# Performance work log

Measured on AMD Instinct MI355X. Metric: run time of the kernel, lower is better.

## Reference

```python
import jax, jax.numpy as jnp
import numpy as np

B, S, D, H = 4, 2048, 1024, 16
HD = D // H


def setup_inputs() -> dict:
    key = jax.random.key(0)
    ks = jax.random.split(key, 9)
    s = 0.02  # GPT-2 init scale for weights
    return {
        "hidden_states": jax.random.normal(ks[0], (B, S, D), jnp.float32),
        "Wq": jax.random.normal(ks[1], (D, D), jnp.float32) * s,
        "bq": jnp.zeros((D,), jnp.float32),
        "Wk": jax.random.normal(ks[2], (D, D), jnp.float32) * s,
        "bk": jnp.zeros((D,), jnp.float32),
        "Wv": jax.random.normal(ks[3], (D, D), jnp.float32) * s,
        "bv": jnp.zeros((D,), jnp.float32),
        "Wo": jax.random.normal(ks[4], (D, D), jnp.float32) * s,
        "bo": jnp.zeros((D,), jnp.float32),
    }


def _split_heads(x):
    b, s, _ = x.shape
    return x.reshape(b, s, H, HD).transpose(0, 2, 1, 3)  # [B,H,S,HD]


def reference(hidden_states, Wq, bq, Wk, bk, Wv, bv, Wo, bo):
    b, s, d = hidden_states.shape
    q = _split_heads(hidden_states @ Wq + bq)
    k = _split_heads(hidden_states @ Wk + bk)
    v = _split_heads(hidden_states @ Wv + bv)
    # naive attention: full [B,H,S,S] scores, scale, causal where-mask, softmax, AV
    scores = jnp.einsum('bhqd,bhkd->bhqk', q, k)
    scores = scores / jnp.asarray(HD, scores.dtype) ** 0.5  # scale_attn_weights
    causal = jnp.tril(jnp.ones((s, s), dtype=bool))  # bias buffer slice
    scores = jnp.where(causal, scores, jnp.finfo(scores.dtype).min)
    attn = jax.nn.softmax(scores, axis=-1)  # attn_dropout p=0 -> identity
    out = jnp.einsum('bhqk,bhkd->bhqd', attn, v)
    out = out.transpose(0, 2, 1, 3).reshape(b, s, d)  # merge heads
    return out @ Wo + bo  # resid_dropout p=0 -> identity
```

## Files before the change

### kernel.cpp

```cpp
#include <hip/hip_runtime.h>
#include <stdint.h>


#define GAS __attribute__((address_space(1)))
#define LAS __attribute__((address_space(3)))

typedef __attribute__((ext_vector_type(4))) float f32x4;
typedef __attribute__((ext_vector_type(8))) short bf16x8;

__device__ __forceinline__ short f2bf(float f) {
  union { float f; uint32_t u; } v; v.f = f;
  uint32_t r = v.u + 0x7fffu + ((v.u >> 16) & 1u);
  return (short)(r >> 16);
}

__device__ __forceinline__ float bf2f(short s) {
  union { uint32_t u; float f; } v;
  v.u = ((uint32_t)(uint16_t)s) << 16;
  return v.f;
}

__device__ __forceinline__ uint32_t cvt_pk_bf16(float lo, float hi) {
  uint32_t r;
  asm("v_cvt_pk_bf16_f32 %0, %1, %2" : "=v"(r) : "v"(lo), "v"(hi));
  return r;
}

__device__ __forceinline__ void gload_lds16(const void* g, void* l) {
  __builtin_amdgcn_global_load_lds((const GAS void*)g, (LAS void*)l, 16, 0, 0);
}

#define GATE(N)                                            \
  __builtin_amdgcn_sched_barrier(0);                       \
  asm volatile("s_waitcnt vmcnt(" #N ")" ::: "memory");    \
  __builtin_amdgcn_s_barrier();                            \
  __builtin_amdgcn_sched_barrier(0);

__global__ __launch_bounds__(256) void cvt_bf16_kernel(const float* __restrict__ in,
                                                       short* __restrict__ out, int n4) {
  int i = blockIdx.x * blockDim.x + threadIdx.x;
  int stride = gridDim.x * blockDim.x;
  for (int idx = i; idx < n4; idx += stride) {
    float4 v = ((const float4*)in)[idx];
    short4 o;
    o.x = f2bf(v.x); o.y = f2bf(v.y); o.z = f2bf(v.z); o.w = f2bf(v.w);
    ((short4*)out)[idx] = o;
  }
}

__global__ __launch_bounds__(256) void wt4_kernel(const float* __restrict__ W0,
                                                  const float* __restrict__ W1,
                                                  const float* __restrict__ W2,
                                                  const float* __restrict__ W3,
                                                  short* __restrict__ Wt) {
  __shared__ short tile[64][65];
  const float* W = (blockIdx.z == 0) ? W0 : (blockIdx.z == 1) ? W1
                   : (blockIdx.z == 2) ? W2 : W3;
  short* dst = Wt + ((size_t)blockIdx.z << 20);
  const int k0 = blockIdx.x * 64, n0 = blockIdx.y * 64;
  const int t = threadIdx.x;
#pragma unroll
  for (int i = 0; i < 16; ++i) {
    int r = (t >> 6) + i * 4, c = t & 63;
    tile[r][c] = f2bf(W[(size_t)(k0 + r) * 1024 + n0 + c]);
  }
  __syncthreads();
#pragma unroll
  for (int i = 0; i < 16; ++i) {
    int r = (t >> 6) + i * 4, c = t & 63;
    dst[(size_t)(n0 + r) * 1024 + k0 + c] = tile[c][r];
  }
}

template <int MODE>
__global__ __launch_bounds__(256, 4) void gemmS(const short* __restrict__ A,
                                                const short* __restrict__ Bt,
                                                const float* __restrict__ b0,
                                                const float* __restrict__ b1,
                                                const float* __restrict__ b2,
                                                void* __restrict__ O0,
                                                void* __restrict__ O1,
                                                void* __restrict__ O2) {
  __shared__ short lds[2][8192];
  const int xcd = (int)blockIdx.x & 7;
  const int t = (int)blockIdx.x >> 3;
  const int m0 = (xcd * 8 + (t & 7)) * 128;
  const int n0 = (t >> 3) * 128;
  const int tid = threadIdx.x;
  const int lane = tid & 63, w = tid >> 6;
  const int l15 = lane & 15, lg = lane >> 4;
  const int wm = w >> 1, wn = w & 1;

  const short* ag[2];
  const short* bg[2];
#pragma unroll
  for (int i = 0; i < 2; ++i) {
    const int P = w * 64 + i * 256 + lane;
    const int L = P ^ ((P >> 3) & 7);
    ag[i] = A + (size_t)(m0 + (L >> 2)) * 1024 + (L & 3) * 8;
    bg[i] = Bt + (size_t)(n0 + (L >> 2)) * 1024 + (L & 3) * 8;
  }

  int aof[4], bof[4];
#pragma unroll
  for (int mf = 0; mf < 4; ++mf) {
    const int L = (wm * 64 + mf * 16 + l15) * 4 + lg;
    aof[mf] = (L ^ ((L >> 3) & 7)) * 8;
  }
#pragma unroll
  for (int nf = 0; nf < 4; ++nf) {
    const int L = (wn * 64 + nf * 16 + l15) * 4 + lg;
    bof[nf] = (L ^ ((L >> 3) & 7)) * 8;
  }

  f32x4 acc[4][4];
#pragma unroll
  for (int i = 0; i < 4; ++i)
#pragma unroll
    for (int j = 0; j < 4; ++j) acc[i][j] = (f32x4){0.f, 0.f, 0.f, 0.f};

  auto stage = [&](int bi, int kt) {
    short* As = &lds[bi][0];
    short* Bs = &lds[bi][4096];
#pragma unroll
    for (int i = 0; i < 2; ++i) {
      gload_lds16(ag[i] + kt * 32, As + (w * 64 + i * 256) * 8);
      gload_lds16(bg[i] + kt * 32, Bs + (w * 64 + i * 256) * 8);
    }
  };

  auto compute = [&](int bi) {
    const short* As = &lds[bi][0];
    const short* Bs = &lds[bi][4096];
    bf16x8 a[4], b[4];
#pragma unroll
    for (int mf = 0; mf < 4; ++mf) a[mf] = *(const bf16x8*)&As[aof[mf]];
#pragma unroll
    for (int nf = 0; nf < 4; ++nf) b[nf] = *(const bf16x8*)&Bs[bof[nf]];
#pragma unroll
    for (int mf = 0; mf < 4; ++mf)
#pragma unroll
      for (int nf = 0; nf < 4; ++nf)
        acc[mf][nf] =
            __builtin_amdgcn_mfma_f32_16x16x32_bf16(a[mf], b[nf], acc[mf][nf], 0, 0, 0);
  };

  stage(0, 0);
  __syncthreads();
  int cur = 0;
  for (int kt = 0; kt < 32; ++kt) {
    if (kt + 1 < 32) stage(cur ^ 1, kt + 1);
    compute(cur);
    __syncthreads();
    cur ^= 1;
  }

  if (MODE == 1) {
    float* dst = (float*)O0;
#pragma unroll
    for (int mf = 0; mf < 4; ++mf)
#pragma unroll
      for (int nf = 0; nf < 4; ++nf) {
        const int col = n0 + wn * 64 + nf * 16 + l15;
        const float bv = b0[col];
#pragma unroll
        for (int rr = 0; rr < 4; ++rr) {
          const int row = m0 + wm * 64 + mf * 16 + lg * 4 + rr;
          dst[(size_t)row * 1024 + col] = acc[mf][nf][rr] + bv;
        }
      }
  } else {
    const int mat = n0 >> 10;
    const int nc0 = n0 & 1023;
    const float* bias = (mat == 0) ? b0 : (mat == 1) ? b1 : b2;
    if (mat < 2) {
      short* dst = (short*)(mat == 0 ? O0 : O1);
#pragma unroll
      for (int mf = 0; mf < 4; ++mf)
#pragma unroll
        for (int nf = 0; nf < 4; ++nf) {
          const int col = nc0 + wn * 64 + nf * 16 + l15;
          const float bv = bias[col];
          const int h = col >> 6, hd = col & 63;
#pragma unroll
          for (int rr = 0; rr < 4; ++rr) {
            const int row = m0 + wm * 64 + mf * 16 + lg * 4 + rr;
            const int b = row >> 11, s = row & 2047;
            dst[((size_t)(b * 16 + h) * 2048 + s) * 64 + hd] = f2bf(acc[mf][nf][rr] + bv);
          }
        }
    } else {
      short* dst = (short*)O2;
#pragma unroll
      for (int mf = 0; mf < 4; ++mf) {
        const int rowb = m0 + wm * 64 + mf * 16 + lg * 4;
        const int b = rowb >> 11, s = rowb & 2047;
        const int s2 = (s & ~31) | (((s >> 2) & 3) << 3) | (((s >> 4) & 1) << 2);
#pragma unroll
        for (int nf = 0; nf < 4; ++nf) {
          const int col = nc0 + wn * 64 + nf * 16 + l15;
          const float bv = bias[col];
          const int h = col >> 6, hd = col & 63;
          short4 sv;
          sv.x = f2bf(acc[mf][nf][0] + bv);
          sv.y = f2bf(acc[mf][nf][1] + bv);
          sv.z = f2bf(acc[mf][nf][2] + bv);
          sv.w = f2bf(acc[mf][nf][3] + bv);
          *(short4*)&dst[((size_t)(b * 16 + h) * 64 + hd) * 2048 + s2] = sv;
        }
      }
    }
  }
}

__global__ __launch_bounds__(256) void attn_kernel(const short* __restrict__ Q,
                                                   const short* __restrict__ K,
                                                   const short* __restrict__ Vt,
                                                   short* __restrict__ Oout) {
  __shared__ short Ks[3][4096];
  __shared__ short Vs[3][4096];
  const int g = (int)blockIdx.x;
  const int bh = (((g >> 3) & 7) << 3) | (g & 7);
  const int jq = 15 - (g >> 6);
  const int q0 = jq * 128;
  const int tid = threadIdx.x;
  const int lane = tid & 63, w = tid >> 6;
  const int l15 = lane & 15, lg = lane >> 4;
  const short* Qb = Q + (size_t)bh * 2048 * 64;
  const short* Kb = K + (size_t)bh * 2048 * 64;
  const short* Vb = Vt + (size_t)bh * 64 * 2048;
  const int b = bh >> 4, h = bh & 15;
  const float SC = 0.18033688011112042f;
  const int qg0 = q0 + w * 32;

  bf16x8 qf[2][2];
#pragma unroll
  for (int qs = 0; qs < 2; ++qs)
#pragma unroll
    for (int kk = 0; kk < 2; ++kk) {
      bf16x8 rq =
          *(const bf16x8*)&Qb[(size_t)(qg0 + qs * 16 + l15) * 64 + kk * 32 + lg * 8];
      union { uint32_t u[4]; bf16x8 v; } sq;
#pragma unroll
      for (int d = 0; d < 4; ++d)
        sq.u[d] = cvt_pk_bf16(bf2f(rq[2 * d]) * SC, bf2f(rq[2 * d + 1]) * SC);
      qf[qs][kk] = sq.v;
    }

  union { short s[8]; bf16x8 v; } one_u;
#pragma unroll
  for (int i = 0; i < 8; ++i) one_u.s[i] = (short)0x3F80;

  const short* kg[2];
  const short* vg[2];
#pragma unroll
  for (int i = 0; i < 2; ++i) {
    const int P = (w * 2 + i) * 64 + lane;
    const int L = P ^ ((P >> 3) & 7);
    kg[i] = Kb + (size_t)(L >> 3) * 64 + (L & 7) * 8;
    vg[i] = Vb + (size_t)(L >> 3) * 2048 + (L & 7) * 8;
  }

  int kcol[2], vcol[2];
#pragma unroll
  for (int kk = 0; kk < 2; ++kk) {
    kcol[kk] = (((kk * 4 + lg) ^ (l15 & 7)) << 3);
    vcol[kk] = kcol[kk];
  }

  f32x4 o[2][4];
#pragma unroll
  for (int i = 0; i < 2; ++i)
#pragma unroll
    for (int j = 0; j < 4; ++j) o[i][j] = (f32x4){0.f, 0.f, 0.f, 0.f};
  f32x4 psacc[2] = {(f32x4){0.f, 0.f, 0.f, 0.f}, (f32x4){0.f, 0.f, 0.f, 0.f}};

  auto stageKV = [&](int bi, int kt) {
#pragma unroll
    for (int i = 0; i < 2; ++i) {
      gload_lds16(kg[i] + (size_t)kt * 4096, &Ks[bi][(w * 2 + i) * 512]);
      gload_lds16(vg[i] + kt * 64, &Vs[bi][(w * 2 + i) * 512]);
    }
  };

  const int nkt = 2 * jq + 2;
  stageKV(0, 0);
  stageKV(1, 1);

  int cur = 0;
  for (int kt = 0; kt < nkt; ++kt) {
    if (kt + 1 < nkt) {
      GATE(4)
    } else {
      GATE(0)
    }
    if (kt + 2 < nkt) {
      int nb = cur + 2; if (nb >= 3) nb -= 3;
      stageKV(nb, kt + 2);
    }

    if (kt * 64 <= qg0 + 31) {
      const short* Kc = &Ks[cur][0];
      const short* Vc = &Vs[cur][0];

      f32x4 sacc[4][2];
#pragma unroll
      for (int t = 0; t < 4; ++t)
#pragma unroll
        for (int qs = 0; qs < 2; ++qs) sacc[t][qs] = (f32x4){0.f, 0.f, 0.f, 0.f};
      __builtin_amdgcn_s_setprio(1);
#pragma unroll
      for (int t = 0; t < 4; ++t) {
        const int krow = (t * 16 + l15) * 64;
#pragma unroll
        for (int kk = 0; kk < 2; ++kk) {
          bf16x8 kf = *(const bf16x8*)&Kc[krow + kcol[kk]];
#pragma unroll
          for (int qs = 0; qs < 2; ++qs)
            sacc[t][qs] = __builtin_amdgcn_mfma_f32_16x16x32_bf16(kf, qf[qs][kk],
                                                                  sacc[t][qs], 0, 0, 0);
        }
      }
      __builtin_amdgcn_s_setprio(0);

      if (kt * 64 + 63 > qg0) {
#pragma unroll
        for (int t = 0; t < 4; ++t)
#pragma unroll
          for (int qs = 0; qs < 2; ++qs)
#pragma unroll
            for (int r = 0; r < 4; ++r) {
              const int kg_ = kt * 64 + t * 16 + lg * 4 + r;
              const int qg = qg0 + qs * 16 + l15;
              if (kg_ > qg) sacc[t][qs][r] = -3e38f;
            }
      }

      bf16x8 pa[2][2];
#pragma unroll
      for (int qs = 0; qs < 2; ++qs) {
#pragma unroll
        for (int t = 0; t < 4; ++t)
#pragma unroll
          for (int r = 0; r < 4; ++r)
            sacc[t][qs][r] = __builtin_amdgcn_exp2f(sacc[t][qs][r]);
#pragma unroll
        for (int kk = 0; kk < 2; ++kk) {
          union { uint32_t u[4]; bf16x8 v; } pw;
          pw.u[0] = cvt_pk_bf16(sacc[2 * kk][qs][0], sacc[2 * kk][qs][1]);
          pw.u[1] = cvt_pk_bf16(sacc[2 * kk][qs][2], sacc[2 * kk][qs][3]);
          pw.u[2] = cvt_pk_bf16(sacc[2 * kk + 1][qs][0], sacc[2 * kk + 1][qs][1]);
          pw.u[3] = cvt_pk_bf16(sacc[2 * kk + 1][qs][2], sacc[2 * kk + 1][qs][3]);
          pa[qs][kk] = pw.v;
        }
      }

      __builtin_amdgcn_s_setprio(1);
#pragma unroll
      for (int ds = 0; ds < 4; ++ds) {
        const int vrow = (ds * 16 + l15) * 64;
#pragma unroll
        for (int kk = 0; kk < 2; ++kk) {
          bf16x8 vf = *(const bf16x8*)&Vc[vrow + vcol[kk]];
#pragma unroll
          for (int qs = 0; qs < 2; ++qs)
            o[qs][ds] = __builtin_amdgcn_mfma_f32_16x16x32_bf16(pa[qs][kk], vf,
                                                                o[qs][ds], 0, 0, 0);
        }
      }
#pragma unroll
      for (int qs = 0; qs < 2; ++qs)
#pragma unroll
        for (int kk = 0; kk < 2; ++kk)
          psacc[qs] = __builtin_amdgcn_mfma_f32_16x16x32_bf16(pa[qs][kk], one_u.v,
                                                              psacc[qs], 0, 0, 0);
      __builtin_amdgcn_s_setprio(0);
    }

    cur = cur + 1 == 3 ? 0 : cur + 1;
  }

#pragma unroll
  for (int qs = 0; qs < 2; ++qs) {
    float inv[4];
#pragma unroll
    for (int r = 0; r < 4; ++r) inv[r] = 1.f / psacc[qs][r];
#pragma unroll
    for (int ds = 0; ds < 4; ++ds)
#pragma unroll
      for (int r = 0; r < 4; ++r) {
        const int qg = q0 + w * 32 + qs * 16 + lg * 4 + r;
        const int col = h * 64 + ds * 16 + l15;
        Oout[((size_t)(b * 2048 + qg)) * 1024 + col] = f2bf(o[qs][ds][r] * inv[r]);
      }
  }
}

extern "C" void kernel_launch(void* const* d_in, const int* in_sizes, int n_in,
                              void* d_out, int out_size, void* d_ws, size_t ws_size,
                              hipStream_t stream) {
  const float* hs = (const float*)d_in[0];
  const float* Wq = (const float*)d_in[1];
  const float* bq = (const float*)d_in[2];
  const float* Wk = (const float*)d_in[3];
  const float* bk = (const float*)d_in[4];
  const float* Wv = (const float*)d_in[5];
  const float* bv = (const float*)d_in[6];
  const float* Wo = (const float*)d_in[7];
  const float* bo = (const float*)d_in[8];

  char* ws = (char*)d_ws;
  short* Xbf = (short*)(ws + 0);
  short* Qb  = (short*)(ws + ((size_t)16 << 20));
  short* Kb  = (short*)(ws + ((size_t)32 << 20));
  short* Vtb = (short*)(ws + ((size_t)48 << 20));
  short* Wts = (short*)(ws + ((size_t)64 << 20));
  short* Wot = Wts + ((size_t)3 << 20);

  cvt_bf16_kernel<<<2048, 256, 0, stream>>>(hs, Xbf, (8192 * 1024) / 4);
  wt4_kernel<<<dim3(16, 16, 4), 256, 0, stream>>>(Wq, Wk, Wv, Wo, Wts);

  gemmS<0><<<1536, 256, 0, stream>>>(Xbf, Wts, bq, bk, bv, Qb, Kb, Vtb);

  attn_kernel<<<1024, 256, 0, stream>>>(Qb, Kb, Vtb, Xbf);

  gemmS<1><<<512, 256, 0, stream>>>(Xbf, Wot, bo, nullptr, nullptr,
                                    (float*)d_out, nullptr, nullptr);
}
```

Baseline: 156.6 us.

## Merge prep kernels, deepen GEMM K-tile, double attention query tile per block

Fuses the activation bf16 conversion and the weight transpose into one prep launch, which removes a kernel launch. Doubles the GEMM K-step to 64 with a new row-wise XOR swizzle, so the loop has half as many barriers, at the cost of twice the LDS and lower occupancy (launch bounds 2). The attention kernel now processes 256 query rows per block (64 per wave) with half the blocks, so each K/V tile staged in LDS is reused across more queries. The price is higher register pressure and coarser causal load balance.

```diff
diff --git a/kernel.cpp b/kernel.cpp
--- a/kernel.cpp
+++ b/kernel.cpp
@@ -36,29 +36,33 @@
   __builtin_amdgcn_s_barrier();                            \
   __builtin_amdgcn_sched_barrier(0);
 
-__global__ __launch_bounds__(256) void cvt_bf16_kernel(const float* __restrict__ in,
-                                                       short* __restrict__ out, int n4) {
-  int i = blockIdx.x * blockDim.x + threadIdx.x;
-  int stride = gridDim.x * blockDim.x;
-  for (int idx = i; idx < n4; idx += stride) {
-    float4 v = ((const float4*)in)[idx];
-    short4 o;
-    o.x = f2bf(v.x); o.y = f2bf(v.y); o.z = f2bf(v.z); o.w = f2bf(v.w);
-    ((short4*)out)[idx] = o;
-  }
-}
-
-__global__ __launch_bounds__(256) void wt4_kernel(const float* __restrict__ W0,
-                                                  const float* __restrict__ W1,
-                                                  const float* __restrict__ W2,
-                                                  const float* __restrict__ W3,
-                                                  short* __restrict__ Wt) {
+__global__ __launch_bounds__(256) void prep_kernel(const float* __restrict__ X,
+                                                   const float* __restrict__ W0,
+                                                   const float* __restrict__ W1,
+                                                   const float* __restrict__ W2,
+                                                   const float* __restrict__ W3,
+                                                   short* __restrict__ Xbf,
+                                                   short* __restrict__ Wt) {
+  const int z = blockIdx.z;
+  const int t = threadIdx.x;
+  if (z == 4) {
+    const int bid = blockIdx.x * 16 + blockIdx.y;
+    const float4* src = (const float4*)X;
+    short4* dst = (short4*)Xbf;
+#pragma unroll
+    for (int i = 0; i < 32; ++i) {
+      const int idx = bid * 8192 + i * 256 + t;
+      float4 v = src[idx];
+      short4 o;
+      o.x = f2bf(v.x); o.y = f2bf(v.y); o.z = f2bf(v.z); o.w = f2bf(v.w);
+      dst[idx] = o;
+    }
+    return;
+  }
   __shared__ short tile[64][65];
-  const float* W = (blockIdx.z == 0) ? W0 : (blockIdx.z == 1) ? W1
-                   : (blockIdx.z == 2) ? W2 : W3;
-  short* dst = Wt + ((size_t)blockIdx.z << 20);
+  const float* W = (z == 0) ? W0 : (z == 1) ? W1 : (z == 2) ? W2 : W3;
+  short* dst = Wt + ((size_t)z << 20);
   const int k0 = blockIdx.x * 64, n0 = blockIdx.y * 64;
-  const int t = threadIdx.x;
 #pragma unroll
   for (int i = 0; i < 16; ++i) {
     int r = (t >> 6) + i * 4, c = t & 63;
@@ -73,7 +77,7 @@
 }
 
 template <int MODE>
-__global__ __launch_bounds__(256, 4) void gemmS(const short* __restrict__ A,
+__global__ __launch_bounds__(256, 2) void gemmS(const short* __restrict__ A,
                                                 const short* __restrict__ Bt,
                                                 const float* __restrict__ b0,
                                                 const float* __restrict__ b1,
@@ -81,7 +85,7 @@
                                                 void* __restrict__ O0,
                                                 void* __restrict__ O1,
                                                 void* __restrict__ O2) {
-  __shared__ short lds[2][8192];
+  __shared__ short lds[2][16384];
   const int xcd = (int)blockIdx.x & 7;
   const int t = (int)blockIdx.x >> 3;
   const int m0 = (xcd * 8 + (t & 7)) * 128;
@@ -91,26 +95,23 @@
   const int l15 = lane & 15, lg = lane >> 4;
   const int wm = w >> 1, wn = w & 1;
 
-  const short* ag[2];
-  const short* bg[2];
-#pragma unroll
-  for (int i = 0; i < 2; ++i) {
-    const int P = w * 64 + i * 256 + lane;
-    const int L = P ^ ((P >> 3) & 7);
-    ag[i] = A + (size_t)(m0 + (L >> 2)) * 1024 + (L & 3) * 8;
-    bg[i] = Bt + (size_t)(n0 + (L >> 2)) * 1024 + (L & 3) * 8;
+  const short* ag[4];
+  const short* bg[4];
+#pragma unroll
+  for (int i = 0; i < 4; ++i) {
+    const int P = i * 256 + w * 64 + lane;
+    const int row = P >> 3, cl = (P & 7) ^ (row & 7);
+    ag[i] = A + (size_t)(m0 + row) * 1024 + cl * 8;
+    bg[i] = Bt + (size_t)(n0 + row) * 1024 + cl * 8;
   }
 
   int aof[4], bof[4];
 #pragma unroll
-  for (int mf = 0; mf < 4; ++mf) {
-    const int L = (wm * 64 + mf * 16 + l15) * 4 + lg;
-    aof[mf] = (L ^ ((L >> 3) & 7)) * 8;
-  }
-#pragma unroll
-  for (int nf = 0; nf < 4; ++nf) {
-    const int L = (wn * 64 + nf * 16 + l15) * 4 + lg;
-    bof[nf] = (L ^ ((L >> 3) & 7)) * 8;
+  for (int f = 0; f < 4; ++f) {
+    const int ra = wm * 64 + f * 16 + l15;
+    aof[f] = ra * 64 + ((lg ^ (ra & 7)) * 8);
+    const int rb = wn * 64 + f * 16 + l15;
+    bof[f] = 8192 + rb * 64 + ((lg ^ (rb & 7)) * 8);
   }
 
   f32x4 acc[4][4];
@@ -120,36 +121,36 @@
     for (int j = 0; j < 4; ++j) acc[i][j] = (f32x4){0.f, 0.f, 0.f, 0.f};
 
   auto stage = [&](int bi, int kt) {
-    short* As = &lds[bi][0];
-    short* Bs = &lds[bi][4096];
-#pragma unroll
-    for (int i = 0; i < 2; ++i) {
-      gload_lds16(ag[i] + kt * 32, As + (w * 64 + i * 256) * 8);
-      gload_lds16(bg[i] + kt * 32, Bs + (w * 64 + i * 256) * 8);
+#pragma unroll
+    for (int i = 0; i < 4; ++i) {
+      gload_lds16(ag[i] + kt * 64, &lds[bi][(i * 256 + w * 64) * 8]);
+      gload_lds16(bg[i] + kt * 64, &lds[bi][8192 + (i * 256 + w * 64) * 8]);
     }
   };
 
   auto compute = [&](int bi) {
-    const short* As = &lds[bi][0];
-    const short* Bs = &lds[bi][4096];
-    bf16x8 a[4], b[4];
-#pragma unroll
-    for (int mf = 0; mf < 4; ++mf) a[mf] = *(const bf16x8*)&As[aof[mf]];
-#pragma unroll
-    for (int nf = 0; nf < 4; ++nf) b[nf] = *(const bf16x8*)&Bs[bof[nf]];
-#pragma unroll
-    for (int mf = 0; mf < 4; ++mf)
-#pragma unroll
-      for (int nf = 0; nf < 4; ++nf)
-        acc[mf][nf] =
-            __builtin_amdgcn_mfma_f32_16x16x32_bf16(a[mf], b[nf], acc[mf][nf], 0, 0, 0);
+    const short* sl = &lds[bi][0];
+#pragma unroll
+    for (int kk = 0; kk < 2; ++kk) {
+      bf16x8 a[4], b[4];
+#pragma unroll
+      for (int mf = 0; mf < 4; ++mf) a[mf] = *(const bf16x8*)&sl[aof[mf] ^ (kk * 32)];
+#pragma unroll
+      for (int nf = 0; nf < 4; ++nf) b[nf] = *(const bf16x8*)&sl[bof[nf] ^ (kk * 32)];
+#pragma unroll
+      for (int mf = 0; mf < 4; ++mf)
+#pragma unroll
+        for (int nf = 0; nf < 4; ++nf)
+          acc[mf][nf] =
+              __builtin_amdgcn_mfma_f32_16x16x32_bf16(a[mf], b[nf], acc[mf][nf], 0, 0, 0);
+    }
   };
 
   stage(0, 0);
   __syncthreads();
   int cur = 0;
-  for (int kt = 0; kt < 32; ++kt) {
-    if (kt + 1 < 32) stage(cur ^ 1, kt + 1);
+  for (int kt = 0; kt < 16; ++kt) {
+    if (kt + 1 < 16) stage(cur ^ 1, kt + 1);
     compute(cur);
     __syncthreads();
     cur ^= 1;
@@ -221,8 +222,8 @@
   __shared__ short Vs[3][4096];
   const int g = (int)blockIdx.x;
   const int bh = (((g >> 3) & 7) << 3) | (g & 7);
-  const int jq = 15 - (g >> 6);
-  const int q0 = jq * 128;
+  const int jq = 7 - (g >> 6);
+  const int q0 = jq * 256;
   const int tid = threadIdx.x;
   const int lane = tid & 63, w = tid >> 6;
   const int l15 = lane & 15, lg = lane >> 4;
@@ -231,11 +232,11 @@
   const short* Vb = Vt + (size_t)bh * 64 * 2048;
   const int b = bh >> 4, h = bh & 15;
   const float SC = 0.18033688011112042f;
-  const int qg0 = q0 + w * 32;
-
-  bf16x8 qf[2][2];
-#pragma unroll
-  for (int qs = 0; qs < 2; ++qs)
+  const int qg0 = q0 + w * 64;
+
+  bf16x8 qf[4][2];
+#pragma unroll
+  for (int qs = 0; qs < 4; ++qs)
 #pragma unroll
     for (int kk = 0; kk < 2; ++kk) {
       bf16x8 rq =
@@ -261,19 +262,19 @@
     vg[i] = Vb + (size_t)(L >> 3) * 2048 + (L & 7) * 8;
   }
 
-  int kcol[2], vcol[2];
-#pragma unroll
-  for (int kk = 0; kk < 2; ++kk) {
+  int kcol[2];
+#pragma unroll
+  for (int kk = 0; kk < 2; ++kk)
     kcol[kk] = (((kk * 4 + lg) ^ (l15 & 7)) << 3);
-    vcol[kk] = kcol[kk];
-  }
-
-  f32x4 o[2][4];
-#pragma unroll
-  for (int i = 0; i < 2; ++i)
+
+  f32x4 o[4][4];
+#pragma unroll
+  for (int i = 0; i < 4; ++i)
 #pragma unroll
     for (int j = 0; j < 4; ++j) o[i][j] = (f32x4){0.f, 0.f, 0.f, 0.f};
-  f32x4 psacc[2] = {(f32x4){0.f, 0.f, 0.f, 0.f}, (f32x4){0.f, 0.f, 0.f, 0.f}};
+  f32x4 psacc[4];
+#pragma unroll
+  for (int i = 0; i < 4; ++i) psacc[i] = (f32x4){0.f, 0.f, 0.f, 0.f};
 
   auto stageKV = [&](int bi, int kt) {
 #pragma unroll
@@ -283,7 +284,7 @@
     }
   };
 
-  const int nkt = 2 * jq + 2;
+  const int nkt = 4 * jq + 4;
   stageKV(0, 0);
   stageKV(1, 1);
 
@@ -299,15 +300,15 @@
       stageKV(nb, kt + 2);
     }
 
-    if (kt * 64 <= qg0 + 31) {
+    if (kt * 64 <= qg0 + 63) {
       const short* Kc = &Ks[cur][0];
       const short* Vc = &Vs[cur][0];
 
-      f32x4 sacc[4][2];
+      f32x4 sacc[4][4];
 #pragma unroll
       for (int t = 0; t < 4; ++t)
 #pragma unroll
-        for (int qs = 0; qs < 2; ++qs) sacc[t][qs] = (f32x4){0.f, 0.f, 0.f, 0.f};
+        for (int qs = 0; qs < 4; ++qs) sacc[t][qs] = (f32x4){0.f, 0.f, 0.f, 0.f};
       __builtin_amdgcn_s_setprio(1);
 #pragma unroll
       for (int t = 0; t < 4; ++t) {
@@ -316,7 +317,7 @@
         for (int kk = 0; kk < 2; ++kk) {
           bf16x8 kf = *(const bf16x8*)&Kc[krow + kcol[kk]];
 #pragma unroll
-          for (int qs = 0; qs < 2; ++qs)
+          for (int qs = 0; qs < 4; ++qs)
             sacc[t][qs] = __builtin_amdgcn_mfma_f32_16x16x32_bf16(kf, qf[qs][kk],
                                                                   sacc[t][qs], 0, 0, 0);
         }
@@ -327,7 +328,7 @@
 #pragma unroll
         for (int t = 0; t < 4; ++t)
 #pragma unroll
-          for (int qs = 0; qs < 2; ++qs)
+          for (int qs = 0; qs < 4; ++qs)
 #pragma unroll
             for (int r = 0; r < 4; ++r) {
               const int kg_ = kt * 64 + t * 16 + lg * 4 + r;
@@ -336,9 +337,9 @@
             }
       }
 
-      bf16x8 pa[2][2];
-#pragma unroll
-      for (int qs = 0; qs < 2; ++qs) {
+      bf16x8 pa[4][2];
+#pragma unroll
+      for (int qs = 0; qs < 4; ++qs) {
 #pragma unroll
         for (int t = 0; t < 4; ++t)
 #pragma unroll
@@ -361,15 +362,15 @@
         const int vrow = (ds * 16 + l15) * 64;
 #pragma unroll
         for (int kk = 0; kk < 2; ++kk) {
-          bf16x8 vf = *(const bf16x8*)&Vc[vrow + vcol[kk]];
-#pragma unroll
-          for (int qs = 0; qs < 2; ++qs)
+          bf16x8 vf = *(const bf16x8*)&Vc[vrow + kcol[kk]];
+#pragma unroll
+          for (int qs = 0; qs < 4; ++qs)
             o[qs][ds] = __builtin_amdgcn_mfma_f32_16x16x32_bf16(pa[qs][kk], vf,
                                                                 o[qs][ds], 0, 0, 0);
         }
       }
 #pragma unroll
-      for (int qs = 0; qs < 2; ++qs)
+      for (int qs = 0; qs < 4; ++qs)
 #pragma unroll
         for (int kk = 0; kk < 2; ++kk)
           psacc[qs] = __builtin_amdgcn_mfma_f32_16x16x32_bf16(pa[qs][kk], one_u.v,
@@ -381,7 +382,7 @@
   }
 
 #pragma unroll
-  for (int qs = 0; qs < 2; ++qs) {
+  for (int qs = 0; qs < 4; ++qs) {
     float inv[4];
 #pragma unroll
     for (int r = 0; r < 4; ++r) inv[r] = 1.f / psacc[qs][r];
@@ -389,7 +390,7 @@
     for (int ds = 0; ds < 4; ++ds)
 #pragma unroll
       for (int r = 0; r < 4; ++r) {
-        const int qg = q0 + w * 32 + qs * 16 + lg * 4 + r;
+        const int qg = qg0 + qs * 16 + lg * 4 + r;
         const int col = h * 64 + ds * 16 + l15;
         Oout[((size_t)(b * 2048 + qg)) * 1024 + col] = f2bf(o[qs][ds][r] * inv[r]);
       }
@@ -417,12 +418,11 @@
   short* Wts = (short*)(ws + ((size_t)64 << 20));
   short* Wot = Wts + ((size_t)3 << 20);
 
-  cvt_bf16_kernel<<<2048, 256, 0, stream>>>(hs, Xbf, (8192 * 1024) / 4);
-  wt4_kernel<<<dim3(16, 16, 4), 256, 0, stream>>>(Wq, Wk, Wv, Wo, Wts);
+  prep_kernel<<<dim3(16, 16, 5), 256, 0, stream>>>(hs, Wq, Wk, Wv, Wo, Xbf, Wts);
 
   gemmS<0><<<1536, 256, 0, stream>>>(Xbf, Wts, bq, bk, bv, Qb, Kb, Vtb);
 
-  attn_kernel<<<1024, 256, 0, stream>>>(Qb, Kb, Vtb, Xbf);
+  attn_kernel<<<512, 256, 0, stream>>>(Qb, Kb, Vtb, Xbf);
 
   gemmS<1><<<512, 256, 0, stream>>>(Xbf, Wot, bo, nullptr, nullptr,
                                     (float*)d_out, nullptr, nullptr);
```

New measurement: 164.9 us. 1.05x slower.
